# Optimization experiments

Measured on AMD Instinct MI355X. Metric: run time of the kernel, lower is better.

The kernel has to match this reference:

```python
import jax, jax.numpy as jnp
import numpy as np

B, T_STEPS, H, W = 8192, 512, 64, 64


def setup_inputs() -> dict:
    key = jax.random.key(0)
    k_w, k_g, k_i, k_j, k_a = jax.random.split(key, 5)
    walls = (jax.random.uniform(k_w, (B, H, W)) < 0.3).astype(jnp.float32)
    walls = walls.at[:, 0, :].set(1.0).at[:, H - 1, :].set(1.0)
    walls = walls.at[:, :, 0].set(1.0).at[:, :, W - 1].set(1.0)
    # goals: sparse cells with value 10 (the code checks goals[...] == 10)
    goals = jnp.where(jax.random.uniform(k_g, (B, H, W)) < 0.02, 10.0, 0.0).astype(jnp.float32)
    # start positions strictly interior; clear the wall at each start cell
    i0 = jax.random.randint(k_i, (B,), 1, H - 1)
    j0 = jax.random.randint(k_j, (B,), 1, W - 1)
    walls = walls.at[jnp.arange(B), i0, j0].set(0.0)
    world = jnp.stack([walls, goals], axis=1)  # [B, 2, H, W]
    s0 = jnp.stack([i0, j0], axis=1).astype(jnp.float32)  # [B, 2]
    a = jax.random.randint(k_a, (B, T_STEPS), 0, 5).astype(jnp.int32)  # actions in {0..4}
    return {"s0": s0, "a": a, "world": world, "T": T_STEPS}


def _rollout(s0, a, world, T):
    walls = world[:, 0].reshape(world.shape[0], -1)  # [B, H*W]
    goals = world[:, 1].reshape(world.shape[0], -1)  # [B, H*W]
    Wd = world.shape[3]

    def step(s, a_t):
        # action deltas: 1 -> row-1, 2 -> row+1, 3 -> col-1, 4 -> col+1, 0 -> stay
        dr = jnp.where(a_t == 1, -1.0, jnp.where(a_t == 2, 1.0, 0.0))
        dc = jnp.where(a_t == 3, -1.0, jnp.where(a_t == 4, 1.0, 0.0))
        s_new = s + jnp.stack([dr, dc], axis=1).astype(s.dtype)  # [B, 2]
        idx = (s_new[:, 0].astype(jnp.int32) * Wd + s_new[:, 1].astype(jnp.int32))[:, None]
        g = jnp.take_along_axis(goals, idx, axis=1)[:, 0]
        w = jnp.take_along_axis(walls, idx, axis=1)[:, 0]
        hit_goal = g == 10.0
        hit_wall = jnp.logical_and(jnp.logical_not(hit_goal), w == 1.0)
        r = jnp.where(hit_goal, 1.0, jnp.where(hit_wall, -1.0, -0.01)).astype(jnp.float32)
        s_next = jnp.where(hit_wall[:, None], s, s_new)  # revert move on wall hit
        return s_next, (s_next, r)

    _, (s_traj, r_traj) = jax.lax.scan(step, s0, jnp.swapaxes(a[:, :T], 0, 1))
    s_full = jnp.concatenate([s0[:, None, :], jnp.swapaxes(s_traj, 0, 1)], axis=1)  # [B, T+1, 2]
    r0 = jnp.zeros((s0.shape[0], 1), dtype=jnp.float32)
    r_full = jnp.concatenate([r0, jnp.swapaxes(r_traj, 0, 1)], axis=1)  # [B, T+1]
    return s_full, r_full


def reference(s0, a, world, T):
    return _rollout(s0, a, world, T)
```

## Files before the change

### kernel.cpp

```cpp
#include <hip/hip_runtime.h>
#include <stdint.h>

#define T_STEPS 512
#define CELLS   4096
#define EPB     32
#define WPE     256
#define WPAD    257

__device__ __forceinline__ uint32_t code4(float4 w, float4 g) {
    uint32_t b0 = (g.x == 10.0f) ? 2u : ((w.x == 1.0f) ? 1u : 0u);
    uint32_t b1 = (g.y == 10.0f) ? 2u : ((w.y == 1.0f) ? 1u : 0u);
    uint32_t b2 = (g.z == 10.0f) ? 2u : ((w.z == 1.0f) ? 1u : 0u);
    uint32_t b3 = (g.w == 10.0f) ? 2u : ((w.w == 1.0f) ? 1u : 0u);
    return b0 | (b1 << 2) | (b2 << 4) | (b3 << 6);
}

__global__ __launch_bounds__(64) void pack_kernel(
    const float* __restrict__ world, uint32_t* __restrict__ packed)
{
    const int b = blockIdx.x;
    const int t = threadIdx.x;
    const float* wbase = world + (size_t)b * (2 * CELLS);
    const float* gbase = wbase + CELLS;
    #pragma unroll
    for (int h = 0; h < 4; ++h) {
        const int w  = h * 64 + t;
        const int c0 = w * 16;
        uint32_t word = 0;
        #pragma unroll
        for (int j = 0; j < 4; ++j) {
            float4 wf = *(const float4*)(wbase + c0 + 4 * j);
            float4 gf = *(const float4*)(gbase + c0 + 4 * j);
            word |= code4(wf, gf) << (8 * j);
        }
        packed[(size_t)b * WPE + w] = word;
    }
}

__global__ __launch_bounds__(64) void rollout_kernel(
    const float* __restrict__ s0,
    const int*   __restrict__ act,
    const uint32_t* __restrict__ packed,
    float* __restrict__ out,
    int B)
{
    __shared__ uint32_t lds[EPB * WPAD];

    const int tid = threadIdx.x;
    const int b0  = blockIdx.x * EPB;

    for (int ee = 0; ee < EPB; ++ee) {
        uint4 v = *(const uint4*)(packed + (size_t)(b0 + ee) * WPE + tid * 4);
        const int base = ee * WPAD + tid * 4;
        lds[base]     = v.x;
        lds[base + 1] = v.y;
        lds[base + 2] = v.z;
        lds[base + 3] = v.w;
    }
    __syncthreads();

    if (tid < EPB) {
        const int b = b0 + tid;
        float2 s = *(const float2*)(s0 + 2 * (size_t)b);
        int r = (int)s.x;
        int c = (int)s.y;
        int p = r * 64 + c;
        const uint32_t* my = lds + tid * WPAD;

        auto lookup = [&](int q) -> int {
            const int idx = q + ((q < 0) ? CELLS : 0);
            const uint32_t wd = my[(idx >> 4) & (WPE - 1)];
            const int cell = (wd >> ((idx & 15) * 2)) & 3;
            return ((unsigned)idx < (unsigned)CELLS) ? cell : 0;
        };

        float* s_out = out + (size_t)b * (2 * (T_STEPS + 1));
        float* r_out = out + (size_t)B * (2 * (T_STEPS + 1)) + (size_t)b * (T_STEPS + 1);

        *(float2*)s_out = s;
        r_out[0] = 0.0f;

        const int4* ap = (const int4*)(act + (size_t)b * T_STEPS);
        int4 A0 = ap[0];
        int4 A1 = ap[1];
        int4 A2 = ap[2];
        for (int k = 0; k < T_STEPS / 4; ++k) {
            const int4 A3 = (k + 3 < T_STEPS / 4) ? ap[k + 3] : A0;
            const int as4[4] = {A0.x, A0.y, A0.z, A0.w};
            #pragma unroll
            for (int jj = 0; jj < 2; ++jj) {
                const int t  = k * 4 + jj * 2;
                const int a0 = as4[2 * jj];
                const int a1 = as4[2 * jj + 1];
                const int d0r = (a0 == 1) ? -1 : ((a0 == 2) ? 1 : 0);
                const int d0c = (a0 == 3) ? -1 : ((a0 == 4) ? 1 : 0);
                const int d1r = (a1 == 1) ? -1 : ((a1 == 2) ? 1 : 0);
                const int d1c = (a1 == 3) ? -1 : ((a1 == 4) ? 1 : 0);
                const int e0 = d0r * 64 + d0c;
                const int e1 = d1r * 64 + d1c;
                const int q0  = p + e0;
                const int q10 = p + e1;
                const int q11 = q0 + e1;
                const int l0  = lookup(q0);
                const int l10 = lookup(q10);
                const int l11 = lookup(q11);
                const bool hw0  = (l0 == 1);
                const float rew0 = (l0 == 2) ? 1.0f : (hw0 ? -1.0f : -0.01f);
                const int p0  = hw0 ? p : q0;
                const int r0v = hw0 ? r : r + d0r;
                const int c0v = hw0 ? c : c + d0c;
                const int l1 = hw0 ? l10 : l11;
                const bool hw1  = (l1 == 1);
                const float rew1 = (l1 == 2) ? 1.0f : (hw1 ? -1.0f : -0.01f);
                p = hw1 ? p0 : p0 + e1;
                r = hw1 ? r0v : r0v + d1r;
                c = hw1 ? c0v : c0v + d1c;
                *(float2*)(s_out + 2 * (t + 1)) = make_float2((float)r0v, (float)c0v);
                *(float2*)(s_out + 2 * (t + 2)) = make_float2((float)r, (float)c);
                r_out[t + 1] = rew0;
                r_out[t + 2] = rew1;
            }
            A0 = A1; A1 = A2; A2 = A3;
        }
    }
}

extern "C" void kernel_launch(void* const* d_in, const int* in_sizes, int n_in,
                              void* d_out, int out_size, void* d_ws, size_t ws_size,
                              hipStream_t stream) {
    const float* s0    = (const float*)d_in[0];
    const int*   act   = (const int*)d_in[1];
    const float* world = (const float*)d_in[2];
    float*       out   = (float*)d_out;
    uint32_t*    packed = (uint32_t*)d_ws;

    const int B = in_sizes[0] / 2;

    pack_kernel<<<B, 64, 0, stream>>>(world, packed);
    rollout_kernel<<<B / EPB, 64, 0, stream>>>(s0, act, packed, out, B);
}
```

Before: 461.8 us.

## Speculatively prefetch all wall outcomes for four steps per LDS batch

Each group of four steps now issues 15 speculative LDS loads, one for every combination of earlier wall hits, before resolving the chain with selects. Before, the speculation covered only two steps at a time. The aim is to shorten the serial chain of dependent LDS-load latencies in the single-wave-per-block rollout. Out-of-range cells are routed to a zeroed padding word instead of being masked after the load. This costs more LDS traffic and VGPR pressure in exchange for fewer load-to-use round trips.

```diff
diff --git a/kernel.cpp b/kernel.cpp
--- a/kernel.cpp
+++ b/kernel.cpp
@@ -57,6 +57,7 @@
         lds[base + 2] = v.z;
         lds[base + 3] = v.w;
     }
+    if (tid < EPB) lds[tid * WPAD + WPE] = 0u;
     __syncthreads();
 
     if (tid < EPB) {
@@ -67,11 +68,9 @@
         int p = r * 64 + c;
         const uint32_t* my = lds + tid * WPAD;
 
-        auto lookup = [&](int q) -> int {
-            const int idx = q + ((q < 0) ? CELLS : 0);
-            const uint32_t wd = my[(idx >> 4) & (WPE - 1)];
-            const int cell = (wd >> ((idx & 15) * 2)) & 3;
-            return ((unsigned)idx < (unsigned)CELLS) ? cell : 0;
+        auto waddr = [&](int q) -> uint32_t {
+            const int u = q + ((q >> 31) & CELLS);
+            return ((unsigned)u < (unsigned)CELLS) ? ((unsigned)u >> 4) : (unsigned)WPE;
         };
 
         float* s_out = out + (size_t)b * (2 * (T_STEPS + 1));
@@ -86,40 +85,81 @@
         int4 A2 = ap[2];
         for (int k = 0; k < T_STEPS / 4; ++k) {
             const int4 A3 = (k + 3 < T_STEPS / 4) ? ap[k + 3] : A0;
-            const int as4[4] = {A0.x, A0.y, A0.z, A0.w};
-            #pragma unroll
-            for (int jj = 0; jj < 2; ++jj) {
-                const int t  = k * 4 + jj * 2;
-                const int a0 = as4[2 * jj];
-                const int a1 = as4[2 * jj + 1];
-                const int d0r = (a0 == 1) ? -1 : ((a0 == 2) ? 1 : 0);
-                const int d0c = (a0 == 3) ? -1 : ((a0 == 4) ? 1 : 0);
-                const int d1r = (a1 == 1) ? -1 : ((a1 == 2) ? 1 : 0);
-                const int d1c = (a1 == 3) ? -1 : ((a1 == 4) ? 1 : 0);
-                const int e0 = d0r * 64 + d0c;
-                const int e1 = d1r * 64 + d1c;
-                const int q0  = p + e0;
-                const int q10 = p + e1;
-                const int q11 = q0 + e1;
-                const int l0  = lookup(q0);
-                const int l10 = lookup(q10);
-                const int l11 = lookup(q11);
-                const bool hw0  = (l0 == 1);
-                const float rew0 = (l0 == 2) ? 1.0f : (hw0 ? -1.0f : -0.01f);
-                const int p0  = hw0 ? p : q0;
-                const int r0v = hw0 ? r : r + d0r;
-                const int c0v = hw0 ? c : c + d0c;
-                const int l1 = hw0 ? l10 : l11;
-                const bool hw1  = (l1 == 1);
-                const float rew1 = (l1 == 2) ? 1.0f : (hw1 ? -1.0f : -0.01f);
-                p = hw1 ? p0 : p0 + e1;
-                r = hw1 ? r0v : r0v + d1r;
-                c = hw1 ? c0v : c0v + d1c;
-                *(float2*)(s_out + 2 * (t + 1)) = make_float2((float)r0v, (float)c0v);
-                *(float2*)(s_out + 2 * (t + 2)) = make_float2((float)r, (float)c);
-                r_out[t + 1] = rew0;
-                r_out[t + 2] = rew1;
-            }
+            const int a0 = A0.x, a1 = A0.y, a2 = A0.z, a3 = A0.w;
+            const int d0r = (a0 == 1) ? -1 : ((a0 == 2) ? 1 : 0);
+            const int d0c = (a0 == 3) ? -1 : ((a0 == 4) ? 1 : 0);
+            const int d1r = (a1 == 1) ? -1 : ((a1 == 2) ? 1 : 0);
+            const int d1c = (a1 == 3) ? -1 : ((a1 == 4) ? 1 : 0);
+            const int d2r = (a2 == 1) ? -1 : ((a2 == 2) ? 1 : 0);
+            const int d2c = (a2 == 3) ? -1 : ((a2 == 4) ? 1 : 0);
+            const int d3r = (a3 == 1) ? -1 : ((a3 == 2) ? 1 : 0);
+            const int d3c = (a3 == 3) ? -1 : ((a3 == 4) ? 1 : 0);
+            const int e0 = d0r * 64 + d0c;
+            const int e1 = d1r * 64 + d1c;
+            const int e2 = d2r * 64 + d2c;
+            const int e3 = d3r * 64 + d3c;
+
+            const uint32_t w0     = my[waddr(p + e0)];
+            const uint32_t w1_0   = my[waddr(p + e1)];
+            const uint32_t w1_1   = my[waddr(p + e0 + e1)];
+            const uint32_t w2_00  = my[waddr(p + e2)];
+            const uint32_t w2_01  = my[waddr(p + e1 + e2)];
+            const uint32_t w2_10  = my[waddr(p + e0 + e2)];
+            const uint32_t w2_11  = my[waddr(p + e0 + e1 + e2)];
+            const uint32_t w3_000 = my[waddr(p + e3)];
+            const uint32_t w3_001 = my[waddr(p + e2 + e3)];
+            const uint32_t w3_010 = my[waddr(p + e1 + e3)];
+            const uint32_t w3_011 = my[waddr(p + e1 + e2 + e3)];
+            const uint32_t w3_100 = my[waddr(p + e0 + e3)];
+            const uint32_t w3_101 = my[waddr(p + e0 + e2 + e3)];
+            const uint32_t w3_110 = my[waddr(p + e0 + e1 + e3)];
+            const uint32_t w3_111 = my[waddr(p + e0 + e1 + e2 + e3)];
+
+            const int t = k * 4;
+
+            int q = p + e0;
+            int u = q + ((q >> 31) & CELLS);
+            int cell = (w0 >> ((u & 15) << 1)) & 3;
+            bool tk0 = (cell != 1);
+            float rew = (cell == 2) ? 1.0f : ((cell == 1) ? -1.0f : -0.01f);
+            p = tk0 ? q : p;  r = tk0 ? r + d0r : r;  c = tk0 ? c + d0c : c;
+            *(float2*)(s_out + 2 * (t + 1)) = make_float2((float)r, (float)c);
+            r_out[t + 1] = rew;
+
+            const uint32_t W1 = tk0 ? w1_1 : w1_0;
+            q = p + e1;
+            u = q + ((q >> 31) & CELLS);
+            cell = (W1 >> ((u & 15) << 1)) & 3;
+            bool tk1 = (cell != 1);
+            rew = (cell == 2) ? 1.0f : ((cell == 1) ? -1.0f : -0.01f);
+            p = tk1 ? q : p;  r = tk1 ? r + d1r : r;  c = tk1 ? c + d1c : c;
+            *(float2*)(s_out + 2 * (t + 2)) = make_float2((float)r, (float)c);
+            r_out[t + 2] = rew;
+
+            const uint32_t W2 = tk0 ? (tk1 ? w2_11 : w2_10)
+                                    : (tk1 ? w2_01 : w2_00);
+            q = p + e2;
+            u = q + ((q >> 31) & CELLS);
+            cell = (W2 >> ((u & 15) << 1)) & 3;
+            bool tk2 = (cell != 1);
+            rew = (cell == 2) ? 1.0f : ((cell == 1) ? -1.0f : -0.01f);
+            p = tk2 ? q : p;  r = tk2 ? r + d2r : r;  c = tk2 ? c + d2c : c;
+            *(float2*)(s_out + 2 * (t + 3)) = make_float2((float)r, (float)c);
+            r_out[t + 3] = rew;
+
+            const uint32_t W3 = tk0 ? (tk1 ? (tk2 ? w3_111 : w3_110)
+                                            : (tk2 ? w3_101 : w3_100))
+                                    : (tk1 ? (tk2 ? w3_011 : w3_010)
+                                            : (tk2 ? w3_001 : w3_000));
+            q = p + e3;
+            u = q + ((q >> 31) & CELLS);
+            cell = (W3 >> ((u & 15) << 1)) & 3;
+            bool tk3 = (cell != 1);
+            rew = (cell == 2) ? 1.0f : ((cell == 1) ? -1.0f : -0.01f);
+            p = tk3 ? q : p;  r = tk3 ? r + d3r : r;  c = tk3 ? c + d3c : c;
+            *(float2*)(s_out + 2 * (t + 4)) = make_float2((float)r, (float)c);
+            r_out[t + 4] = rew;
+
             A0 = A1; A1 = A2; A2 = A3;
         }
     }
```

Measured after the change: 515.0 us. 1.12x slower.
